# Kernel optimization log

Hardware: AMD Instinct MI355X
Metric: run time of the kernel (lower is better)

## Reference

```python
import jax, jax.numpy as jnp
import numpy as np

N, E, V_IN, HID, U_IN, B, MEM = 50000, 800000, 128, 128, 64, 64, 128
CAT = V_IN + HID + U_IN  # 320 == hidden*2 + u_in
ALPHA = 0.5
EPS = 1e-5


def setup_inputs() -> dict:
    key = jax.random.key(0)
    ks = jax.random.split(key, 12)
    x = jax.random.normal(ks[0], (N, V_IN), dtype=jnp.float32)
    edge_index = jax.random.randint(ks[1], (2, E), 0, N, dtype=jnp.int64)
    edge_attr = jax.random.normal(ks[2], (E, HID), dtype=jnp.float32)
    u = jax.random.normal(ks[3], (B, U_IN), dtype=jnp.float32)
    batch = jnp.sort(jax.random.randint(ks[4], (N,), 0, B, dtype=jnp.int64))
    Mk = jax.random.normal(ks[5], (MEM, CAT), dtype=jnp.float32)
    Mv = jax.random.normal(ks[6], (MEM, CAT), dtype=jnp.float32)
    ln_gamma = jnp.ones((CAT,), dtype=jnp.float32)
    ln_beta = jnp.zeros((CAT,), dtype=jnp.float32)
    W1 = jax.random.normal(ks[7], (CAT, HID), dtype=jnp.float32) * (1.0 / np.sqrt(CAT))
    b1 = jnp.zeros((HID,), dtype=jnp.float32)
    W2 = jax.random.normal(ks[8], (HID, HID), dtype=jnp.float32) * (1.0 / np.sqrt(HID))
    b2 = jnp.zeros((HID,), dtype=jnp.float32)
    return {"x": x, "edge_index": edge_index, "edge_attr": edge_attr, "u": u,
            "batch": batch, "Mk": Mk, "Mv": Mv, "ln_gamma": ln_gamma,
            "ln_beta": ln_beta, "W1": W1, "b1": b1, "W2": W2, "b2": b2}


def reference(x, edge_index, edge_attr, u, batch, Mk, Mv, ln_gamma, ln_beta, W1, b1, W2, b2):
    # scatter_add over destination nodes
    agg = jax.ops.segment_sum(edge_attr, edge_index[1], num_segments=N)  # [N, HID]
    out = jnp.concatenate([x, agg, u[batch]], axis=1)  # [N, CAT]
    # LayerNorm over last dim
    mu = jnp.mean(out, axis=-1, keepdims=True)
    var = jnp.var(out, axis=-1, keepdims=True)
    out = (out - mu) * jax.lax.rsqrt(var + EPS) * ln_gamma + ln_beta
    # External attention: [N,CAT] @ [CAT,MEM] -> softmax over MEM -> @ [MEM,CAT]
    scores = jnp.einsum('nc,mc->nm', out, Mk)
    attn = jax.nn.softmax(scores, axis=-1)
    attn_out = jnp.einsum('nm,mc->nc', attn, Mv)
    out = ALPHA * attn_out + (1.0 - ALPHA) * out
    # MLP
    h = jax.nn.relu(out @ W1 + b1)
    return h @ W2 + b2
```

## Files before the change

kernel.cpp:

```cpp
#include <hip/hip_runtime.h>

#define NN   50000
#define EE   800000
#define VIN  128
#define HIDN 128
#define UIN  64
#define MEMN 128
#define CATN 320
#define LN_EPS 1e-5f
#define SCAN_NB 196

typedef __attribute__((ext_vector_type(8))) short short8;
typedef __attribute__((ext_vector_type(4))) float f32x4;
typedef __attribute__((ext_vector_type(4))) unsigned int uint4v;
typedef __attribute__((ext_vector_type(4))) unsigned short ushort4v;
typedef unsigned short ushort_t;

__device__ inline ushort_t f32_bf16(float f) {
    unsigned u = __float_as_uint(f);
    return (ushort_t)((u + 0x7FFFu + ((u >> 16) & 1u)) >> 16);
}
__device__ inline float bf16_f32(ushort_t h) {
    return __uint_as_float(((unsigned)h) << 16);
}
__device__ inline unsigned pack_hl(float y) {
    unsigned u  = __float_as_uint(y);
    unsigned hi = (u + 0x7FFFu + ((u >> 16) & 1u)) & 0xFFFF0000u;
    float    lo = y - __uint_as_float(hi);
    unsigned v  = __float_as_uint(lo);
    unsigned l16 = ((v + 0x7FFFu + ((v >> 16) & 1u)) >> 16) & 0xFFFFu;
    return hi | l16;
}

__global__ void hist_kernel(const int* __restrict__ edge_dst, int* __restrict__ count)
{
    int gid = blockIdx.x * 256 + threadIdx.x;
    if (gid < EE) atomicAdd(&count[edge_dst[gid]], 1);
}

__global__ void block_sum_kernel(const int* __restrict__ count, int* __restrict__ partials)
{
    __shared__ int s[256];
    const int tid = threadIdx.x;
    const int gid = blockIdx.x * 256 + tid;
    s[tid] = (gid < NN) ? count[gid] : 0;
    __syncthreads();
    for (int off = 128; off >= 1; off >>= 1) {
        if (tid < off) s[tid] += s[tid + off];
        __syncthreads();
    }
    if (tid == 0) partials[blockIdx.x] = s[0];
}

__global__ void scan_partials_kernel(int* __restrict__ partials)
{
    __shared__ int s[256];
    const int tid = threadIdx.x;
    const int v = (tid < SCAN_NB) ? partials[tid] : 0;
    s[tid] = v;
    __syncthreads();
    for (int off = 1; off < 256; off <<= 1) {
        int t = (tid >= off) ? s[tid - off] : 0;
        __syncthreads();
        s[tid] += t;
        __syncthreads();
    }
    if (tid < SCAN_NB) partials[tid] = s[tid] - v;
}

__global__ void make_offsets_kernel(const int* __restrict__ count,
                                    const int* __restrict__ partials,
                                    int* __restrict__ offsets)
{
    __shared__ int s[256];
    const int tid = threadIdx.x;
    const int gid = blockIdx.x * 256 + tid;
    const int v = (gid < NN) ? count[gid] : 0;
    s[tid] = v;
    __syncthreads();
    for (int off = 1; off < 256; off <<= 1) {
        int t = (tid >= off) ? s[tid - off] : 0;
        __syncthreads();
        s[tid] += t;
        __syncthreads();
    }
    if (gid < NN) offsets[gid] = partials[blockIdx.x] + s[tid] - v;
}

__global__ void fill_kernel(const int* __restrict__ edge_dst,
                            const int* __restrict__ offsets,
                            int* __restrict__ cursor,
                            int* __restrict__ bucket)
{
    int gid = blockIdx.x * 256 + threadIdx.x;
    if (gid >= EE) return;
    const int d = edge_dst[gid];
    const int p = atomicAdd(&cursor[d], 1);
    bucket[offsets[d] + p] = gid;
}

__global__ void prep_all_kernel(const float* __restrict__ Mk,
                                const float* __restrict__ Mv,
                                const float* __restrict__ W1,
                                const float* __restrict__ W2,
                                ushort_t* __restrict__ mk_hi,
                                ushort_t* __restrict__ mk_lo,
                                ushort_t* __restrict__ mv_t,
                                ushort_t* __restrict__ w1_t,
                                ushort_t* __restrict__ w2_t)
{
    int i = blockIdx.x * 256 + threadIdx.x;
    if (i < MEMN * CATN) {
        const float f = Mk[i];
        const ushort_t h = f32_bf16(f);
        mk_hi[i] = h;
        mk_lo[i] = f32_bf16(f - bf16_f32(h));
    }
    if (i < CATN * MEMN) {
        const int c = i >> 7, m = i & 127;
        mv_t[i] = f32_bf16(Mv[m * CATN + c]);
    }
    if (i < HIDN * CATN) {
        const int n = i / CATN, k = i - n * CATN;
        w1_t[i] = f32_bf16(W1[k * HIDN + n]);
    }
    if (i < HIDN * HIDN) {
        const int n = i >> 7, k = i & 127;
        w2_t[i] = f32_bf16(W2[k * HIDN + n]);
    }
}

__global__ __launch_bounds__(256) void gather_ln_kernel(
    const float* __restrict__ edge_attr,
    const int*   __restrict__ bucket,
    const int*   __restrict__ offsets,
    const int*   __restrict__ count,
    const float* __restrict__ x,
    const float* __restrict__ u,
    const int*   __restrict__ batch,
    const float* __restrict__ gamma,
    const float* __restrict__ beta,
    unsigned*    __restrict__ ln_pk)
{
    const int wid  = (blockIdx.x * 256 + threadIdx.x) >> 6;
    const int lane = threadIdx.x & 63;
    if (wid >= NN) return;

    const int start = offsets[wid];
    const int deg   = count[wid];
    const float2* ea2 = reinterpret_cast<const float2*>(edge_attr);
    float2 a = make_float2(0.f, 0.f);
    int i = 0;
    const int d4 = deg & ~3;
    for (; i < d4; i += 4) {
        const int e0 = bucket[start + i];
        const int e1 = bucket[start + i + 1];
        const int e2 = bucket[start + i + 2];
        const int e3 = bucket[start + i + 3];
        const float2 v0 = ea2[(size_t)e0 * 64 + lane];
        const float2 v1 = ea2[(size_t)e1 * 64 + lane];
        const float2 v2 = ea2[(size_t)e2 * 64 + lane];
        const float2 v3 = ea2[(size_t)e3 * 64 + lane];
        a.x += (v0.x + v1.x) + (v2.x + v3.x);
        a.y += (v0.y + v1.y) + (v2.y + v3.y);
    }
    for (; i < deg; ++i) {
        const int e = bucket[start + i];
        const float2 v = ea2[(size_t)e * 64 + lane];
        a.x += v.x;
        a.y += v.y;
    }
    const float2 xv = reinterpret_cast<const float2*>(x)[(size_t)wid * 64 + lane];
    const float  uv = u[batch[wid] * UIN + lane];

    float s = xv.x + xv.y + a.x + a.y + uv;
    float q = xv.x * xv.x + xv.y * xv.y + a.x * a.x + a.y * a.y + uv * uv;
    #pragma unroll
    for (int off = 32; off >= 1; off >>= 1) {
        s += __shfl_xor(s, off);
        q += __shfl_xor(q, off);
    }
    const float mu  = s * (1.0f / CATN);
    const float var = q * (1.0f / CATN) - mu * mu;
    const float rs  = rsqrtf(var + LN_EPS);

    const float2 g0 = reinterpret_cast<const float2*>(gamma)[lane];
    const float2 g1 = reinterpret_cast<const float2*>(gamma)[64 + lane];
    const float  g2 = gamma[256 + lane];
    const float2 t0 = reinterpret_cast<const float2*>(beta)[lane];
    const float2 t1 = reinterpret_cast<const float2*>(beta)[64 + lane];
    const float  t2 = beta[256 + lane];

    unsigned* row = ln_pk + (size_t)wid * CATN;
    uint2 p01, p23;
    p01.x = pack_hl((xv.x - mu) * rs * g0.x + t0.x);
    p01.y = pack_hl((xv.y - mu) * rs * g0.y + t0.y);
    p23.x = pack_hl((a.x - mu) * rs * g1.x + t1.x);
    p23.y = pack_hl((a.y - mu) * rs * g1.y + t1.y);
    reinterpret_cast<uint2*>(row)[lane]       = p01;
    reinterpret_cast<uint2*>(row + 128)[lane] = p23;
    row[256 + lane] = pack_hl((uv - mu) * rs * g2 + t2);
}

#define MSTR 328
#define PSTR 136

__global__ __launch_bounds__(256) void node_mfma_kernel(
    const unsigned* __restrict__ ln_pk,
    const ushort_t* __restrict__ mk_hi,
    const ushort_t* __restrict__ mk_lo,
    const ushort_t* __restrict__ mv_t,
    const ushort_t* __restrict__ w1_t,
    const ushort_t* __restrict__ w2_t,
    const float*    __restrict__ b1,
    const float*    __restrict__ b2,
    float*          __restrict__ out)
{
    __shared__ __align__(16) ushort_t s_lnh[32 * MSTR];
    __shared__ __align__(16) ushort_t s_lnl[32 * MSTR];
    __shared__ __align__(16) ushort_t s_P[32 * PSTR];
    __shared__ __align__(16) float2   s_part[8 * 16];

    const int tid  = threadIdx.x;
    const int wv   = tid >> 6;
    const int lane = tid & 63;
    const int l15  = lane & 15;
    const int l4   = lane >> 4;
    const int node0 = blockIdx.x * 32;

    const f32x4 zero4 = {0.f, 0.f, 0.f, 0.f};

    for (int j = tid; j < 32 * 80; j += 256) {
        const int nl = j / 80;
        const int c0 = (j - nl * 80) * 4;
        int ng = node0 + nl; ng = (ng < NN) ? ng : (NN - 1);
        const uint4v p = *(const uint4v*)(ln_pk + (size_t)ng * CATN + c0);
        ushort4v h4, l4v;
        h4.x = (ushort_t)(p.x >> 16);  l4v.x = (ushort_t)(p.x & 0xFFFFu);
        h4.y = (ushort_t)(p.y >> 16);  l4v.y = (ushort_t)(p.y & 0xFFFFu);
        h4.z = (ushort_t)(p.z >> 16);  l4v.z = (ushort_t)(p.z & 0xFFFFu);
        h4.w = (ushort_t)(p.w >> 16);  l4v.w = (ushort_t)(p.w & 0xFFFFu);
        *(ushort4v*)(s_lnh + nl * MSTR + c0) = h4;
        *(ushort4v*)(s_lnl + nl * MSTR + c0) = l4v;
    }
    __syncthreads();

    {
        f32x4 acc[2][2];
        #pragma unroll
        for (int ai = 0; ai < 2; ++ai)
            #pragma unroll
            for (int bt = 0; bt < 2; ++bt) acc[ai][bt] = zero4;

        #pragma unroll 2
        for (int kc = 0; kc < 10; ++kc) {
            const int koff = kc * 32 + l4 * 8;
            short8 amh[2], aml[2], bnh[2], bnl[2];
            #pragma unroll
            for (int ai = 0; ai < 2; ++ai) {
                const int mr = (wv * 2 + ai) * 16 + l15;
                amh[ai] = *(const short8*)(mk_hi + (size_t)mr * CATN + koff);
                aml[ai] = *(const short8*)(mk_lo + (size_t)mr * CATN + koff);
            }
            #pragma unroll
            for (int bt = 0; bt < 2; ++bt) {
                bnh[bt] = *(const short8*)(s_lnh + (bt * 16 + l15) * MSTR + koff);
                bnl[bt] = *(const short8*)(s_lnl + (bt * 16 + l15) * MSTR + koff);
            }
            #pragma unroll
            for (int ai = 0; ai < 2; ++ai)
                #pragma unroll
                for (int bt = 0; bt < 2; ++bt) {
                    acc[ai][bt] = __builtin_amdgcn_mfma_f32_16x16x32_bf16(amh[ai], bnh[bt], acc[ai][bt], 0, 0, 0);
                    acc[ai][bt] = __builtin_amdgcn_mfma_f32_16x16x32_bf16(aml[ai], bnh[bt], acc[ai][bt], 0, 0, 0);
                    acc[ai][bt] = __builtin_amdgcn_mfma_f32_16x16x32_bf16(amh[ai], bnl[bt], acc[ai][bt], 0, 0, 0);
                }
        }

        #pragma unroll
        for (int bt = 0; bt < 2; ++bt) {
            float mx = acc[0][bt][0];
            #pragma unroll
            for (int ai = 0; ai < 2; ++ai)
                #pragma unroll
                for (int r = 0; r < 4; ++r) mx = fmaxf(mx, acc[ai][bt][r]);
            mx = fmaxf(mx, __shfl_xor(mx, 16));
            mx = fmaxf(mx, __shfl_xor(mx, 32));
            float sm = 0.f;
            #pragma unroll
            for (int ai = 0; ai < 2; ++ai)
                #pragma unroll
                for (int r = 0; r < 4; ++r) sm += __expf(acc[ai][bt][r] - mx);
            sm += __shfl_xor(sm, 16);
            sm += __shfl_xor(sm, 32);
            if (l4 == 0) s_part[(wv * 2 + bt) * 16 + l15] = make_float2(mx, sm);
        }
        __syncthreads();
        #pragma unroll
        for (int bt = 0; bt < 2; ++bt) {
            const float2 p0 = s_part[(0 * 2 + bt) * 16 + l15];
            const float2 p1 = s_part[(1 * 2 + bt) * 16 + l15];
            const float2 p2 = s_part[(2 * 2 + bt) * 16 + l15];
            const float2 p3 = s_part[(3 * 2 + bt) * 16 + l15];
            const float mg = fmaxf(fmaxf(p0.x, p1.x), fmaxf(p2.x, p3.x));
            const float sg = p0.y * __expf(p0.x - mg) + p1.y * __expf(p1.x - mg)
                           + p2.y * __expf(p2.x - mg) + p3.y * __expf(p3.x - mg);
            const float inv = 1.f / sg;
            ushort_t* prow = s_P + (bt * 16 + l15) * PSTR + (wv * 2) * 16 + l4 * 4;
            #pragma unroll
            for (int ai = 0; ai < 2; ++ai)
                #pragma unroll
                for (int r = 0; r < 4; ++r)
                    prow[ai * 16 + r] = f32_bf16(__expf(acc[ai][bt][r] - mg) * inv);
        }
    }
    __syncthreads();

    {
        f32x4 acc[2][5];
        #pragma unroll
        for (int mt = 0; mt < 2; ++mt)
            #pragma unroll
            for (int nn = 0; nn < 5; ++nn) acc[mt][nn] = zero4;

        #pragma unroll
        for (int kc = 0; kc < 4; ++kc) {
            const int koff = kc * 32 + l4 * 8;
            short8 ap[2];
            #pragma unroll
            for (int mt = 0; mt < 2; ++mt)
                ap[mt] = *(const short8*)(s_P + (mt * 16 + l15) * PSTR + koff);
            short8 bv[5];
            #pragma unroll
            for (int nn = 0; nn < 5; ++nn) {
                const int c = (wv * 5 + nn) * 16 + l15;
                bv[nn] = *(const short8*)(mv_t + (size_t)c * MEMN + koff);
            }
            #pragma unroll
            for (int mt = 0; mt < 2; ++mt)
                #pragma unroll
                for (int nn = 0; nn < 5; ++nn)
                    acc[mt][nn] = __builtin_amdgcn_mfma_f32_16x16x32_bf16(ap[mt], bv[nn], acc[mt][nn], 0, 0, 0);
        }
        #pragma unroll
        for (int mt = 0; mt < 2; ++mt)
            #pragma unroll
            for (int nn = 0; nn < 5; ++nn)
                #pragma unroll
                for (int r = 0; r < 4; ++r) {
                    const int node_l = mt * 16 + l4 * 4 + r;
                    const int c = (wv * 5 + nn) * 16 + l15;
                    const int idx = node_l * MSTR + c;
                    const float lnv = bf16_f32(s_lnh[idx]) + bf16_f32(s_lnl[idx]);
                    s_lnh[idx] = f32_bf16(0.5f * (acc[mt][nn][r] + lnv));
                }
    }
    __syncthreads();

    {
        f32x4 acc[2][2];
        #pragma unroll
        for (int mt = 0; mt < 2; ++mt)
            #pragma unroll
            for (int nt = 0; nt < 2; ++nt) acc[mt][nt] = zero4;

        #pragma unroll 2
        for (int kc = 0; kc < 10; ++kc) {
            const int koff = kc * 32 + l4 * 8;
            short8 am[2], bw[2];
            #pragma unroll
            for (int mt = 0; mt < 2; ++mt)
                am[mt] = *(const short8*)(s_lnh + (mt * 16 + l15) * MSTR + koff);
            #pragma unroll
            for (int nt = 0; nt < 2; ++nt) {
                const int n = (wv * 2 + nt) * 16 + l15;
                bw[nt] = *(const short8*)(w1_t + (size_t)n * CATN + koff);
            }
            #pragma unroll
            for (int mt = 0; mt < 2; ++mt)
                #pragma unroll
                for (int nt = 0; nt < 2; ++nt)
                    acc[mt][nt] = __builtin_amdgcn_mfma_f32_16x16x32_bf16(am[mt], bw[nt], acc[mt][nt], 0, 0, 0);
        }
        float bb[2];
        #pragma unroll
        for (int nt = 0; nt < 2; ++nt) bb[nt] = b1[(wv * 2 + nt) * 16 + l15];
        __syncthreads();
        #pragma unroll
        for (int mt = 0; mt < 2; ++mt)
            #pragma unroll
            for (int nt = 0; nt < 2; ++nt)
                #pragma unroll
                for (int r = 0; r < 4; ++r) {
                    const int node_l = mt * 16 + l4 * 4 + r;
                    const int col = (wv * 2 + nt) * 16 + l15;
                    s_P[node_l * PSTR + col] = f32_bf16(fmaxf(acc[mt][nt][r] + bb[nt], 0.f));
                }
    }
    __syncthreads();

    {
        f32x4 acc[2][2];
        #pragma unroll
        for (int mt = 0; mt < 2; ++mt)
            #pragma unroll
            for (int nt = 0; nt < 2; ++nt) acc[mt][nt] = zero4;

        #pragma unroll
        for (int kc = 0; kc < 4; ++kc) {
            const int koff = kc * 32 + l4 * 8;
            short8 ah[2], bw[2];
            #pragma unroll
            for (int mt = 0; mt < 2; ++mt)
                ah[mt] = *(const short8*)(s_P + (mt * 16 + l15) * PSTR + koff);
            #pragma unroll
            for (int nt = 0; nt < 2; ++nt) {
                const int n = (wv * 2 + nt) * 16 + l15;
                bw[nt] = *(const short8*)(w2_t + (size_t)n * HIDN + koff);
            }
            #pragma unroll
            for (int mt = 0; mt < 2; ++mt)
                #pragma unroll
                for (int nt = 0; nt < 2; ++nt)
                    acc[mt][nt] = __builtin_amdgcn_mfma_f32_16x16x32_bf16(ah[mt], bw[nt], acc[mt][nt], 0, 0, 0);
        }
        float bb[2];
        #pragma unroll
        for (int nt = 0; nt < 2; ++nt) bb[nt] = b2[(wv * 2 + nt) * 16 + l15];
        #pragma unroll
        for (int mt = 0; mt < 2; ++mt)
            #pragma unroll
            for (int nt = 0; nt < 2; ++nt)
                #pragma unroll
                for (int r = 0; r < 4; ++r) {
                    const int ng = node0 + mt * 16 + l4 * 4 + r;
                    if (ng < NN) {
                        const int col = (wv * 2 + nt) * 16 + l15;
                        out[(size_t)ng * HIDN + col] = acc[mt][nt][r] + bb[nt];
                    }
                }
    }
}

extern "C" void kernel_launch(void* const* d_in, const int* in_sizes, int n_in,
                              void* d_out, int out_size, void* d_ws, size_t ws_size,
                              hipStream_t stream)
{
    const float* x         = (const float*)d_in[0];
    const int*   edge_idx  = (const int*)  d_in[1];
    const float* edge_attr = (const float*)d_in[2];
    const float* u         = (const float*)d_in[3];
    const int*   batch     = (const int*)  d_in[4];
    const float* Mk        = (const float*)d_in[5];
    const float* Mv        = (const float*)d_in[6];
    const float* gamma     = (const float*)d_in[7];
    const float* beta      = (const float*)d_in[8];
    const float* W1        = (const float*)d_in[9];
    const float* b1        = (const float*)d_in[10];
    const float* W2        = (const float*)d_in[11];
    const float* b2        = (const float*)d_in[12];
    float*       out       = (float*)d_out;

    char* w = (char*)d_ws;
    int*   count     = (int*)w;        w += (size_t)NN * sizeof(int);
    int*   cursor    = (int*)w;        w += (size_t)NN * sizeof(int);
    int*   offsets   = (int*)w;        w += (size_t)NN * sizeof(int);
    int*   partials  = (int*)w;        w += 256 * sizeof(int);
    int*   bucket    = (int*)w;        w += (size_t)EE * sizeof(int);
    w = (char*)(((size_t)w + 255) & ~(size_t)255);
    unsigned* ln_pk  = (unsigned*)w;   w += (size_t)NN * CATN * sizeof(unsigned);
    ushort_t* mk_hi  = (ushort_t*)w;   w += (size_t)MEMN * CATN * 2;
    ushort_t* mk_lo  = (ushort_t*)w;   w += (size_t)MEMN * CATN * 2;
    ushort_t* mv_t   = (ushort_t*)w;   w += (size_t)CATN * MEMN * 2;
    ushort_t* w1_t   = (ushort_t*)w;   w += (size_t)HIDN * CATN * 2;
    ushort_t* w2_t   = (ushort_t*)w;   w += (size_t)HIDN * HIDN * 2;

    const int* edge_dst = edge_idx + EE;

    hipMemsetAsync(count, 0, (size_t)2 * NN * sizeof(int), stream);

    const int eb = (EE + 255) / 256;
    hist_kernel<<<eb, 256, 0, stream>>>(edge_dst, count);
    block_sum_kernel<<<SCAN_NB, 256, 0, stream>>>(count, partials);
    scan_partials_kernel<<<1, 256, 0, stream>>>(partials);
    make_offsets_kernel<<<SCAN_NB, 256, 0, stream>>>(count, partials, offsets);
    fill_kernel<<<eb, 256, 0, stream>>>(edge_dst, offsets, cursor, bucket);

    prep_all_kernel<<<(HIDN * CATN + 255) / 256, 256, 0, stream>>>(
        Mk, Mv, W1, W2, mk_hi, mk_lo, mv_t, w1_t, w2_t);

    gather_ln_kernel<<<(NN * 64 + 255) / 256, 256, 0, stream>>>(
        edge_attr, bucket, offsets, count, x, u, batch, gamma, beta, ln_pk);

    node_mfma_kernel<<<(NN + 31) / 32, 256, 0, stream>>>(
        ln_pk, mk_hi, mk_lo, mv_t, w1_t, w2_t, b1, b2, out);
}
```

Before: 294.8 us.

## Split node MFMA kernel work across 8 wavefronts per 32-node block

The node kernel now runs 512 threads (8 waves) per block instead of 4 waves. Each GEMM stage's per-wave tile work is halved: the scores stage gives each wave 16 memory rows, and the later stages split node tiles by wave parity. The softmax reduction combines 8 partial maxima and sums. An extra barrier is added before the residual writeback, since other waves may still be reading the LN tile. The aim is more waves in flight and lower per-wave latency, at the cost of more barrier overhead and duplicated B-operand loads across waves.

After: 324.0 us. +9.9%, slower.

```diff
diff --git a/kernel.cpp b/kernel.cpp
--- a/kernel.cpp
+++ b/kernel.cpp
@@ -205,7 +205,7 @@
 #define MSTR 328
 #define PSTR 136
 
-__global__ __launch_bounds__(256) void node_mfma_kernel(
+__global__ __launch_bounds__(512) void node_mfma_kernel(
     const unsigned* __restrict__ ln_pk,
     const ushort_t* __restrict__ mk_hi,
     const ushort_t* __restrict__ mk_lo,
@@ -219,7 +219,7 @@
     __shared__ __align__(16) ushort_t s_lnh[32 * MSTR];
     __shared__ __align__(16) ushort_t s_lnl[32 * MSTR];
     __shared__ __align__(16) ushort_t s_P[32 * PSTR];
-    __shared__ __align__(16) float2   s_part[8 * 16];
+    __shared__ __align__(16) float2   s_part[16 * 16];
 
     const int tid  = threadIdx.x;
     const int wv   = tid >> 6;
@@ -230,7 +230,7 @@
 
     const f32x4 zero4 = {0.f, 0.f, 0.f, 0.f};
 
-    for (int j = tid; j < 32 * 80; j += 256) {
+    for (int j = tid; j < 32 * 80; j += 512) {
         const int nl = j / 80;
         const int c0 = (j - nl * 80) * 4;
         int ng = node0 + nl; ng = (ng < NN) ? ng : (NN - 1);
@@ -246,51 +246,39 @@
     __syncthreads();
 
     {
-        f32x4 acc[2][2];
-        #pragma unroll
-        for (int ai = 0; ai < 2; ++ai)
-            #pragma unroll
-            for (int bt = 0; bt < 2; ++bt) acc[ai][bt] = zero4;
+        f32x4 acc[2];
+        acc[0] = zero4; acc[1] = zero4;
 
         #pragma unroll 2
         for (int kc = 0; kc < 10; ++kc) {
             const int koff = kc * 32 + l4 * 8;
-            short8 amh[2], aml[2], bnh[2], bnl[2];
-            #pragma unroll
-            for (int ai = 0; ai < 2; ++ai) {
-                const int mr = (wv * 2 + ai) * 16 + l15;
-                amh[ai] = *(const short8*)(mk_hi + (size_t)mr * CATN + koff);
-                aml[ai] = *(const short8*)(mk_lo + (size_t)mr * CATN + koff);
-            }
+            const int mr = wv * 16 + l15;
+            short8 amh = *(const short8*)(mk_hi + (size_t)mr * CATN + koff);
+            short8 aml = *(const short8*)(mk_lo + (size_t)mr * CATN + koff);
+            short8 bnh[2], bnl[2];
             #pragma unroll
             for (int bt = 0; bt < 2; ++bt) {
                 bnh[bt] = *(const short8*)(s_lnh + (bt * 16 + l15) * MSTR + koff);
                 bnl[bt] = *(const short8*)(s_lnl + (bt * 16 + l15) * MSTR + koff);
             }
             #pragma unroll
-            for (int ai = 0; ai < 2; ++ai)
-                #pragma unroll
-                for (int bt = 0; bt < 2; ++bt) {
-                    acc[ai][bt] = __builtin_amdgcn_mfma_f32_16x16x32_bf16(amh[ai], bnh[bt], acc[ai][bt], 0, 0, 0);
-                    acc[ai][bt] = __builtin_amdgcn_mfma_f32_16x16x32_bf16(aml[ai], bnh[bt], acc[ai][bt], 0, 0, 0);
-                    acc[ai][bt] = __builtin_amdgcn_mfma_f32_16x16x32_bf16(amh[ai], bnl[bt], acc[ai][bt], 0, 0, 0);
-                }
+            for (int bt = 0; bt < 2; ++bt) {
+                acc[bt] = __builtin_amdgcn_mfma_f32_16x16x32_bf16(amh, bnh[bt], acc[bt], 0, 0, 0);
+                acc[bt] = __builtin_amdgcn_mfma_f32_16x16x32_bf16(aml, bnh[bt], acc[bt], 0, 0, 0);
+                acc[bt] = __builtin_amdgcn_mfma_f32_16x16x32_bf16(amh, bnl[bt], acc[bt], 0, 0, 0);
+            }
         }
 
         #pragma unroll
         for (int bt = 0; bt < 2; ++bt) {
-            float mx = acc[0][bt][0];
-            #pragma unroll
-            for (int ai = 0; ai < 2; ++ai)
-                #pragma unroll
-                for (int r = 0; r < 4; ++r) mx = fmaxf(mx, acc[ai][bt][r]);
+            float mx = acc[bt][0];
+            #pragma unroll
+            for (int r = 1; r < 4; ++r) mx = fmaxf(mx, acc[bt][r]);
             mx = fmaxf(mx, __shfl_xor(mx, 16));
             mx = fmaxf(mx, __shfl_xor(mx, 32));
             float sm = 0.f;
             #pragma unroll
-            for (int ai = 0; ai < 2; ++ai)
-                #pragma unroll
-                for (int r = 0; r < 4; ++r) sm += __expf(acc[ai][bt][r] - mx);
+            for (int r = 0; r < 4; ++r) sm += __expf(acc[bt][r] - mx);
             sm += __shfl_xor(sm, 16);
             sm += __shfl_xor(sm, 32);
             if (l4 == 0) s_part[(wv * 2 + bt) * 16 + l15] = make_float2(mx, sm);
@@ -298,147 +286,128 @@
         __syncthreads();
         #pragma unroll
         for (int bt = 0; bt < 2; ++bt) {
-            const float2 p0 = s_part[(0 * 2 + bt) * 16 + l15];
-            const float2 p1 = s_part[(1 * 2 + bt) * 16 + l15];
-            const float2 p2 = s_part[(2 * 2 + bt) * 16 + l15];
-            const float2 p3 = s_part[(3 * 2 + bt) * 16 + l15];
-            const float mg = fmaxf(fmaxf(p0.x, p1.x), fmaxf(p2.x, p3.x));
-            const float sg = p0.y * __expf(p0.x - mg) + p1.y * __expf(p1.x - mg)
-                           + p2.y * __expf(p2.x - mg) + p3.y * __expf(p3.x - mg);
+            float mg = -1e30f;
+            float2 pw[8];
+            #pragma unroll
+            for (int w = 0; w < 8; ++w) {
+                pw[w] = s_part[(w * 2 + bt) * 16 + l15];
+                mg = fmaxf(mg, pw[w].x);
+            }
+            float sg = 0.f;
+            #pragma unroll
+            for (int w = 0; w < 8; ++w) sg += pw[w].y * __expf(pw[w].x - mg);
             const float inv = 1.f / sg;
-            ushort_t* prow = s_P + (bt * 16 + l15) * PSTR + (wv * 2) * 16 + l4 * 4;
-            #pragma unroll
-            for (int ai = 0; ai < 2; ++ai)
-                #pragma unroll
-                for (int r = 0; r < 4; ++r)
-                    prow[ai * 16 + r] = f32_bf16(__expf(acc[ai][bt][r] - mg) * inv);
+            ushort_t* prow = s_P + (bt * 16 + l15) * PSTR + wv * 16 + l4 * 4;
+            #pragma unroll
+            for (int r = 0; r < 4; ++r)
+                prow[r] = f32_bf16(__expf(acc[bt][r] - mg) * inv);
         }
     }
     __syncthreads();
 
     {
-        f32x4 acc[2][5];
-        #pragma unroll
-        for (int mt = 0; mt < 2; ++mt)
-            #pragma unroll
-            for (int nn = 0; nn < 5; ++nn) acc[mt][nn] = zero4;
+        const int mt = wv & 1;
+        const int cg = wv >> 1;
+        f32x4 acc[5];
+        #pragma unroll
+        for (int nn = 0; nn < 5; ++nn) acc[nn] = zero4;
 
         #pragma unroll
         for (int kc = 0; kc < 4; ++kc) {
             const int koff = kc * 32 + l4 * 8;
-            short8 ap[2];
-            #pragma unroll
-            for (int mt = 0; mt < 2; ++mt)
-                ap[mt] = *(const short8*)(s_P + (mt * 16 + l15) * PSTR + koff);
+            short8 ap = *(const short8*)(s_P + (mt * 16 + l15) * PSTR + koff);
             short8 bv[5];
             #pragma unroll
             for (int nn = 0; nn < 5; ++nn) {
-                const int c = (wv * 5 + nn) * 16 + l15;
+                const int c = (cg * 5 + nn) * 16 + l15;
                 bv[nn] = *(const short8*)(mv_t + (size_t)c * MEMN + koff);
             }
             #pragma unroll
-            for (int mt = 0; mt < 2; ++mt)
-                #pragma unroll
-                for (int nn = 0; nn < 5; ++nn)
-                    acc[mt][nn] = __builtin_amdgcn_mfma_f32_16x16x32_bf16(ap[mt], bv[nn], acc[mt][nn], 0, 0, 0);
-        }
-        #pragma unroll
-        for (int mt = 0; mt < 2; ++mt)
-            #pragma unroll
             for (int nn = 0; nn < 5; ++nn)
-                #pragma unroll
-                for (int r = 0; r < 4; ++r) {
-                    const int node_l = mt * 16 + l4 * 4 + r;
-                    const int c = (wv * 5 + nn) * 16 + l15;
-                    const int idx = node_l * MSTR + c;
-                    const float lnv = bf16_f32(s_lnh[idx]) + bf16_f32(s_lnl[idx]);
-                    s_lnh[idx] = f32_bf16(0.5f * (acc[mt][nn][r] + lnv));
-                }
+                acc[nn] = __builtin_amdgcn_mfma_f32_16x16x32_bf16(ap, bv[nn], acc[nn], 0, 0, 0);
+        }
+        __syncthreads();
+        #pragma unroll
+        for (int nn = 0; nn < 5; ++nn)
+            #pragma unroll
+            for (int r = 0; r < 4; ++r) {
+                const int node_l = mt * 16 + l4 * 4 + r;
+                const int c = (cg * 5 + nn) * 16 + l15;
+                const int idx = node_l * MSTR + c;
+                const float lnv = bf16_f32(s_lnh[idx]) + bf16_f32(s_lnl[idx]);
+                s_lnh[idx] = f32_bf16(0.5f * (acc[nn][r] + lnv));
+            }
     }
     __syncthreads();
 
     {
-        f32x4 acc[2][2];
-        #pragma unroll
-        for (int mt = 0; mt < 2; ++mt)
-            #pragma unroll
-            for (int nt = 0; nt < 2; ++nt) acc[mt][nt] = zero4;
+        const int mt  = wv & 1;
+        const int ng2 = wv >> 1;
+        f32x4 acc[2];
+        acc[0] = zero4; acc[1] = zero4;
 
         #pragma unroll 2
         for (int kc = 0; kc < 10; ++kc) {
             const int koff = kc * 32 + l4 * 8;
-            short8 am[2], bw[2];
-            #pragma unroll
-            for (int mt = 0; mt < 2; ++mt)
-                am[mt] = *(const short8*)(s_lnh + (mt * 16 + l15) * MSTR + koff);
+            short8 am = *(const short8*)(s_lnh + (mt * 16 + l15) * MSTR + koff);
+            short8 bw[2];
             #pragma unroll
             for (int nt = 0; nt < 2; ++nt) {
-                const int n = (wv * 2 + nt) * 16 + l15;
+                const int n = (ng2 * 2 + nt) * 16 + l15;
                 bw[nt] = *(const short8*)(w1_t + (size_t)n * CATN + koff);
             }
             #pragma unroll
-            for (int mt = 0; mt < 2; ++mt)
-                #pragma unroll
-                for (int nt = 0; nt < 2; ++nt)
-                    acc[mt][nt] = __builtin_amdgcn_mfma_f32_16x16x32_bf16(am[mt], bw[nt], acc[mt][nt], 0, 0, 0);
+            for (int nt = 0; nt < 2; ++nt)
+                acc[nt] = __builtin_amdgcn_mfma_f32_16x16x32_bf16(am, bw[nt], acc[nt], 0, 0, 0);
         }
         float bb[2];
         #pragma unroll
-        for (int nt = 0; nt < 2; ++nt) bb[nt] = b1[(wv * 2 + nt) * 16 + l15];
-        __syncthreads();
-        #pragma unroll
-        for (int mt = 0; mt < 2; ++mt)
-            #pragma unroll
-            for (int nt = 0; nt < 2; ++nt)
-                #pragma unroll
-                for (int r = 0; r < 4; ++r) {
-                    const int node_l = mt * 16 + l4 * 4 + r;
-                    const int col = (wv * 2 + nt) * 16 + l15;
-                    s_P[node_l * PSTR + col] = f32_bf16(fmaxf(acc[mt][nt][r] + bb[nt], 0.f));
-                }
+        for (int nt = 0; nt < 2; ++nt) bb[nt] = b1[(ng2 * 2 + nt) * 16 + l15];
+        __syncthreads();
+        #pragma unroll
+        for (int nt = 0; nt < 2; ++nt)
+            #pragma unroll
+            for (int r = 0; r < 4; ++r) {
+                const int node_l = mt * 16 + l4 * 4 + r;
+                const int col = (ng2 * 2 + nt) * 16 + l15;
+                s_P[node_l * PSTR + col] = f32_bf16(fmaxf(acc[nt][r] + bb[nt], 0.f));
+            }
     }
     __syncthreads();
 
     {
-        f32x4 acc[2][2];
-        #pragma unroll
-        for (int mt = 0; mt < 2; ++mt)
-            #pragma unroll
-            for (int nt = 0; nt < 2; ++nt) acc[mt][nt] = zero4;
+        const int mt  = wv & 1;
+        const int ng2 = wv >> 1;
+        f32x4 acc[2];
+        acc[0] = zero4; acc[1] = zero4;
 
         #pragma unroll
         for (int kc = 0; kc < 4; ++kc) {
             const int koff = kc * 32 + l4 * 8;
-            short8 ah[2], bw[2];
-            #pragma unroll
-            for (int mt = 0; mt < 2; ++mt)
-                ah[mt] = *(const short8*)(s_P + (mt * 16 + l15) * PSTR + koff);
+            short8 ah = *(const short8*)(s_P + (mt * 16 + l15) * PSTR + koff);
+            short8 bw[2];
             #pragma unroll
             for (int nt = 0; nt < 2; ++nt) {
-                const int n = (wv * 2 + nt) * 16 + l15;
+                const int n = (ng2 * 2 + nt) * 16 + l15;
                 bw[nt] = *(const short8*)(w2_t + (size_t)n * HIDN + koff);
             }
             #pragma unroll
-            for (int mt = 0; mt < 2; ++mt)
-                #pragma unroll
-                for (int nt = 0; nt < 2; ++nt)
-                    acc[mt][nt] = __builtin_amdgcn_mfma_f32_16x16x32_bf16(ah[mt], bw[nt], acc[mt][nt], 0, 0, 0);
+            for (int nt = 0; nt < 2; ++nt)
+                acc[nt] = __builtin_amdgcn_mfma_f32_16x16x32_bf16(ah, bw[nt], acc[nt], 0, 0, 0);
         }
         float bb[2];
         #pragma unroll
-        for (int nt = 0; nt < 2; ++nt) bb[nt] = b2[(wv * 2 + nt) * 16 + l15];
-        #pragma unroll
-        for (int mt = 0; mt < 2; ++mt)
-            #pragma unroll
-            for (int nt = 0; nt < 2; ++nt)
-                #pragma unroll
-                for (int r = 0; r < 4; ++r) {
-                    const int ng = node0 + mt * 16 + l4 * 4 + r;
-                    if (ng < NN) {
-                        const int col = (wv * 2 + nt) * 16 + l15;
-                        out[(size_t)ng * HIDN + col] = acc[mt][nt][r] + bb[nt];
-                    }
+        for (int nt = 0; nt < 2; ++nt) bb[nt] = b2[(ng2 * 2 + nt) * 16 + l15];
+        #pragma unroll
+        for (int nt = 0; nt < 2; ++nt)
+            #pragma unroll
+            for (int r = 0; r < 4; ++r) {
+                const int ng = node0 + (wv & 1) * 16 + l4 * 4 + r;
+                if (ng < NN) {
+                    const int col = (ng2 * 2 + nt) * 16 + l15;
+                    out[(size_t)ng * HIDN + col] = acc[nt][r] + bb[nt];
                 }
+            }
     }
 }
 
@@ -492,6 +461,6 @@
     gather_ln_kernel<<<(NN * 64 + 255) / 256, 256, 0, stream>>>(
         edge_attr, bucket, offsets, count, x, u, batch, gamma, beta, ln_pk);
 
-    node_mfma_kernel<<<(NN + 31) / 32, 256, 0, stream>>>(
+    node_mfma_kernel<<<(NN + 31) / 32, 512, 0, stream>>>(
         ln_pk, mk_hi, mk_lo, mv_t, w1_t, w2_t, b1, b2, out);
 }
```
